# Kernel tuning notes

Hardware: AMD Instinct MI355X
Metric: run time of the kernel (lower is better)

Reference implementation:

```python
import jax, jax.numpy as jnp
import numpy as np

DIM = 1024
HEADS = 16
DIM_HEAD = 64
INNER = HEADS * DIM_HEAD  # 1024
EPS = 1e-5


def layernorm(x, w, b):
    mu = jnp.mean(x, axis=-1, keepdims=True)
    var = jnp.mean(jnp.square(x - mu), axis=-1, keepdims=True)
    return (x - mu) * jax.lax.rsqrt(var + EPS) * w + b


def setup_inputs() -> dict:
    key = jax.random.key(0)
    ks = jax.random.split(key, 9)
    b, n1, n2 = 4, 4096, 256
    x = jax.random.normal(ks[0], (b, n1, DIM), dtype=jnp.float32)
    latents = jax.random.normal(ks[1], (b, n2, DIM), dtype=jnp.float32)
    shift = jax.random.normal(ks[2], (b, HEADS), dtype=jnp.float32)
    scale = jax.random.normal(ks[3], (b, HEADS), dtype=jnp.float32)
    s = 1.0 / np.sqrt(DIM)
    Wq = jax.random.normal(ks[4], (DIM, INNER), dtype=jnp.float32) * s
    Wkv = jax.random.normal(ks[5], (DIM, 2 * INNER), dtype=jnp.float32) * s
    Wout = jax.random.normal(ks[6], (INNER, DIM), dtype=jnp.float32) * (1.0 / np.sqrt(INNER))
    ln1_w = jnp.ones((DIM,), jnp.float32)
    ln1_b = jnp.zeros((DIM,), jnp.float32)
    ln2_w = jnp.ones((DIM,), jnp.float32)
    ln2_b = jnp.zeros((DIM,), jnp.float32)
    return {"x": x, "latents": latents, "shift": shift, "scale": scale,
            "ln1_w": ln1_w, "ln1_b": ln1_b, "ln2_w": ln2_w, "ln2_b": ln2_b,
            "Wq": Wq, "Wkv": Wkv, "Wout": Wout}


def reference(x, latents, shift, scale, ln1_w, ln1_b, ln2_w, ln2_b, Wq, Wkv, Wout):
    b = x.shape[0]
    xn = layernorm(x, ln1_w, ln1_b)            # (b, n1, D)
    ln = layernorm(latents, ln2_w, ln2_b)      # (b, n2, D)
    q = ln @ Wq                                 # (b, n2, inner)
    kv = xn @ Wkv                               # (b, n1, 2*inner)
    k, v = jnp.split(kv, 2, axis=-1)
    q = q.reshape(b, -1, HEADS, DIM_HEAD)
    k = k.reshape(b, -1, HEADS, DIM_HEAD)
    v = v.reshape(b, -1, HEADS, DIM_HEAD)
    # AdaLN-style per-head modulation on q
    q = q * (1.0 + scale[:, None, :, None]) + shift[:, None, :, None]
    # fp32 attention scores (already fp32 here)
    attn_scale = DIM_HEAD ** -0.5
    qk = jnp.einsum('bihd,bjhd->bhij', q.astype(jnp.float32), k.astype(jnp.float32)) * attn_scale
    attn = jax.nn.softmax(qk, axis=-1).astype(v.dtype)  # (b, h, n2, n1)
    out = jnp.einsum('bhij,bjhd->bihd', attn, v)         # (b, n2, h, dh)
    out = out.reshape(b, -1, INNER)
    return out @ Wout
```

## Files before the change

kernel.cpp:

```cpp
#include <hip/hip_runtime.h>

typedef __bf16 bf16;
typedef bf16 bf16x8 __attribute__((ext_vector_type(8)));
typedef bf16 bf16x4 __attribute__((ext_vector_type(4)));
typedef float f32x4 __attribute__((ext_vector_type(4)));

#define B_ 4
#define N1 4096
#define N2 256
#define DIM 1024
#define HEADS 16
#define DH 64
#define INNER 1024
#define ASPLIT 4
#define KEYS_PER_SPLIT (N1 / ASPLIT)
#define SPLIT_ELEMS (4 * 16 * 256 * 64)
#define ROWS_TOTAL (4 * HEADS * N2)

typedef __attribute__((address_space(1))) const void gvoid_t;
typedef __attribute__((address_space(3))) void lvoid_t;
__device__ __forceinline__ void async16(const void* g, void* l) {
  __builtin_amdgcn_global_load_lds((gvoid_t*)g, (lvoid_t*)l, 16, 0, 0);
}

__global__ __launch_bounds__(256) void prep(
    const float* __restrict__ Wq, const float* __restrict__ Wkv,
    const float* __restrict__ Wout, bf16* __restrict__ WqT,
    bf16* __restrict__ WkvT, bf16* __restrict__ WoutT,
    const float* __restrict__ x, const float* __restrict__ latents,
    const float* __restrict__ ln1w, const float* __restrict__ ln1b,
    const float* __restrict__ ln2w, const float* __restrict__ ln2b,
    bf16* __restrict__ xn, bf16* __restrict__ lnl) {
  __shared__ float tile[32][33];
  int t = blockIdx.x;
  if (t < 4096) {
    const float* src;
    bf16* dst;
    int N;
    if (t < 1024) { src = Wq; dst = WqT; N = 1024; }
    else if (t < 3072) { t -= 1024; src = Wkv; dst = WkvT; N = 2048; }
    else { t -= 3072; src = Wout; dst = WoutT; N = 1024; }
    int ntiles = N >> 5;
    int n0 = (t % ntiles) * 32, k0 = (t / ntiles) * 32;
    int xx = threadIdx.x & 31, yy = threadIdx.x >> 5;
    for (int j = 0; j < 4; j++)
      tile[yy + 8 * j][xx] = src[(size_t)(k0 + yy + 8 * j) * N + n0 + xx];
    __syncthreads();
    for (int j = 0; j < 4; j++)
      dst[(size_t)(n0 + yy + 8 * j) * 1024 + k0 + xx] = (bf16)tile[xx][yy + 8 * j];
    return;
  }
  int wv = threadIdx.x >> 6, lane = threadIdx.x & 63;
  int grow = (t - 4096) * 4 + wv;
  const float *src, *w, *bb;
  bf16* dst;
  int row;
  if (grow < 16384) { src = x; w = ln1w; bb = ln1b; dst = xn; row = grow; }
  else { src = latents; w = ln2w; bb = ln2b; dst = lnl; row = grow - 16384; }
  const float4* p = (const float4*)(src + (size_t)row * DIM);
  float4 v[4];
  for (int j = 0; j < 4; j++) v[j] = p[j * 64 + lane];
  float s = 0.f, sq = 0.f;
  for (int j = 0; j < 4; j++) {
    s += v[j].x + v[j].y + v[j].z + v[j].w;
    sq += v[j].x * v[j].x + v[j].y * v[j].y + v[j].z * v[j].z + v[j].w * v[j].w;
  }
  for (int off = 32; off; off >>= 1) {
    s += __shfl_xor(s, off, 64);
    sq += __shfl_xor(sq, off, 64);
  }
  float mu = s * (1.0f / DIM);
  float var = sq * (1.0f / DIM) - mu * mu;
  float r = rsqrtf(var + 1e-5f);
  for (int j = 0; j < 4; j++) {
    float4 wv4 = ((const float4*)w)[j * 64 + lane];
    float4 bv4 = ((const float4*)bb)[j * 64 + lane];
    bf16x4 o;
    o[0] = (bf16)((v[j].x - mu) * r * wv4.x + bv4.x);
    o[1] = (bf16)((v[j].y - mu) * r * wv4.y + bv4.y);
    o[2] = (bf16)((v[j].z - mu) * r * wv4.z + bv4.z);
    o[3] = (bf16)((v[j].w - mu) * r * wv4.w + bv4.w);
    *(bf16x4*)(dst + (size_t)row * DIM + (j * 64 + lane) * 4) = o;
  }
}

__device__ __forceinline__ int swz_off(int row, int cb) {
  int line = row >> 1;
  return (line << 7) + (((((row & 1) << 2) | cb) ^ (line & 7)) << 4);
}

__global__ __launch_bounds__(512, 2) void gemm_kv256(
    const bf16* __restrict__ A, const bf16* __restrict__ Bt,
    bf16* __restrict__ Cout, bf16* __restrict__ Cout2) {
  extern __shared__ char smem[];
  int tid = threadIdx.x;
  int lane = tid & 63, wv = tid >> 6;
  int lr = lane & 15, quad = lane >> 4;
  int wr = wv >> 2, wc = wv & 3;
  int bid = blockIdx.x;
  int mt = (bid & 7) * 8 + ((bid >> 3) >> 3), nt = (bid >> 3) & 7;
  int m0 = mt * 256, n0 = nt * 256;

  int offA[8], offB[4];
#pragma unroll
  for (int im = 0; im < 8; im++) offA[im] = swz_off(wr * 128 + im * 16 + lr, quad);
#pragma unroll
  for (int in = 0; in < 4; in++) offB[in] = swz_off(wc * 64 + in * 16 + lr, quad);

  size_t gA[2], gB[2];
#pragma unroll
  for (int s = 0; s < 2; s++) {
    int u = s * 512 + tid;
    int line = u >> 3, inner = (u & 7) ^ (line & 7);
    int row = line * 2 + (inner >> 2), cb = inner & 3;
    gA[s] = (size_t)(m0 + row) * 1024 + cb * 8;
    gB[s] = (size_t)(n0 + row) * 1024 + cb * 8;
  }
  int ldsS0 = wv * 1024, ldsS1 = 8192 + wv * 1024;

  auto stA = [&](int b, int kh, int k0) {
    char* base = smem + b * 32768 + kh * 16384;
    async16(&A[gA[0] + k0], base + ldsS0);
    async16(&A[gA[1] + k0], base + ldsS1);
  };
  auto stB = [&](int b, int kh, int k0) {
    char* base = smem + 65536 + b * 32768 + kh * 16384;
    async16(&Bt[gB[0] + k0], base + ldsS0);
    async16(&Bt[gB[1] + k0], base + ldsS1);
  };

  f32x4 acc[8][4] = {};

  stA(0, 0, 0);  stB(0, 0, 0);
  stA(0, 1, 32); stB(0, 1, 32);
  stA(1, 0, 64); stB(1, 0, 64);
  asm volatile("s_waitcnt vmcnt(4)" ::: "memory");
  __builtin_amdgcn_s_barrier();

#pragma unroll 1
  for (int t = 0; t < 16; t++) {
    int b = t & 1;
    const char* A0 = smem + b * 32768;
    const char* A1 = A0 + 16384;
    const char* B0 = smem + 65536 + b * 32768;
    const char* B1 = B0 + 16384;
    int k1 = (t + 1 < 16 ? t + 1 : 15) * 64;
    int k2 = (t + 2 < 16 ? t + 2 : 15) * 64;
    bf16x8 af[4], bfr[4];
#pragma unroll
    for (int in = 0; in < 4; in++) bfr[in] = *(const bf16x8*)(B0 + offB[in]);
#pragma unroll
    for (int im = 0; im < 4; im++) af[im] = *(const bf16x8*)(A0 + offA[im]);
    stA(b ^ 1, 1, k1 + 32);
    __builtin_amdgcn_s_barrier();
    __builtin_amdgcn_s_setprio(1);
#pragma unroll
    for (int im = 0; im < 4; im++)
#pragma unroll
      for (int in = 0; in < 4; in++)
        acc[im][in] = __builtin_amdgcn_mfma_f32_16x16x32_bf16(
            af[im], bfr[in], acc[im][in], 0, 0, 0);
    __builtin_amdgcn_s_setprio(0);
    __builtin_amdgcn_s_barrier();
#pragma unroll
    for (int im = 0; im < 4; im++) af[im] = *(const bf16x8*)(A0 + offA[4 + im]);
    stB(b ^ 1, 1, k1 + 32);
    __builtin_amdgcn_s_barrier();
    __builtin_amdgcn_s_setprio(1);
#pragma unroll
    for (int im = 0; im < 4; im++)
#pragma unroll
      for (int in = 0; in < 4; in++)
        acc[4 + im][in] = __builtin_amdgcn_mfma_f32_16x16x32_bf16(
            af[im], bfr[in], acc[4 + im][in], 0, 0, 0);
    __builtin_amdgcn_s_setprio(0);
    __builtin_amdgcn_s_barrier();
#pragma unroll
    for (int in = 0; in < 4; in++) bfr[in] = *(const bf16x8*)(B1 + offB[in]);
#pragma unroll
    for (int im = 0; im < 4; im++) af[im] = *(const bf16x8*)(A1 + offA[im]);
    stA(b, 0, k2);
    __builtin_amdgcn_s_barrier();
    __builtin_amdgcn_s_setprio(1);
#pragma unroll
    for (int im = 0; im < 4; im++)
#pragma unroll
      for (int in = 0; in < 4; in++)
        acc[im][in] = __builtin_amdgcn_mfma_f32_16x16x32_bf16(
            af[im], bfr[in], acc[im][in], 0, 0, 0);
    __builtin_amdgcn_s_setprio(0);
    __builtin_amdgcn_s_barrier();
#pragma unroll
    for (int im = 0; im < 4; im++) af[im] = *(const bf16x8*)(A1 + offA[4 + im]);
    stB(b, 0, k2);
    __builtin_amdgcn_s_barrier();
    __builtin_amdgcn_s_setprio(1);
#pragma unroll
    for (int im = 0; im < 4; im++)
#pragma unroll
      for (int in = 0; in < 4; in++)
        acc[4 + im][in] = __builtin_amdgcn_mfma_f32_16x16x32_bf16(
            af[im], bfr[in], acc[4 + im][in], 0, 0, 0);
    __builtin_amdgcn_s_setprio(0);
    asm volatile("s_waitcnt vmcnt(4)" ::: "memory");
    __builtin_amdgcn_s_barrier();
  }

  asm volatile("s_waitcnt vmcnt(0)" ::: "memory");
  __builtin_amdgcn_s_barrier();

  if (n0 < 1024) {
#pragma unroll
    for (int im = 0; im < 8; im++)
#pragma unroll
      for (int in = 0; in < 4; in++) {
        int col = n0 + wc * 64 + in * 16 + lr;
#pragma unroll
        for (int r = 0; r < 4; r++) {
          int row = m0 + wr * 128 + im * 16 + quad * 4 + r;
          Cout[(size_t)row * 1024 + col] = (bf16)acc[im][in][r];
        }
      }
    return;
  }
  int b2 = m0 >> 12;
  int key0 = (m0 & 4095) + wr * 128;
  int gc0 = (n0 - 1024) + wc * 64;
  bf16* Tw = (bf16*)(smem + wv * 8704);
  for (int pass = 0; pass < 2; pass++) {
#pragma unroll
    for (int ii = 0; ii < 2; ii++) {
      int in = pass * 2 + ii;
      int cl = ii * 16 + lr;
#pragma unroll
      for (int im = 0; im < 8; im++) {
        bf16x4 pk;
#pragma unroll
        for (int r = 0; r < 4; r++) pk[r] = (bf16)acc[im][in][r];
        *(bf16x4*)&Tw[cl * 136 + im * 16 + quad * 4] = pk;
      }
    }
    asm volatile("s_waitcnt lgkmcnt(0)" ::: "memory");
#pragma unroll
    for (int j = 0; j < 8; j++) {
      int idx = j * 64 + lane;
      int cl = idx >> 4, k8 = idx & 15;
      uint4 val = *(const uint4*)&Tw[cl * 136 + k8 * 8];
      *(uint4*)&Cout2[((size_t)(b2 * 1024 + gc0 + pass * 32 + cl)) * 4096 +
                      key0 + k8 * 8] = val;
    }
    asm volatile("s_waitcnt lgkmcnt(0)" ::: "memory");
  }
}

template <int MODE>
__global__ __launch_bounds__(256) void gemm64(
    const bf16* __restrict__ A, const bf16* __restrict__ Bt,
    void* __restrict__ Cout, int K, int N,
    const float* __restrict__ shiftp, const float* __restrict__ scalep) {
  __shared__ __align__(16) bf16 As[3][64 * 64];
  __shared__ __align__(16) bf16 Bs[3][64 * 64];
  int tid = threadIdx.x;
  int lane = tid & 63, wv = tid >> 6;
  int wr = wv >> 1, wc = wv & 1;
  int quad = lane >> 4, lr = lane & 15;
  int m0 = blockIdx.y * 64, n0 = blockIdx.x * 64;
  f32x4 acc[2][2] = {};

  auto stage = [&](int step, int buf) {
    int kt = step * 64;
    for (int j = 0; j < 2; j++) {
      int idx0 = j * 256 + wv * 64;
      int row = (idx0 >> 3) + (lane >> 3);
      int cb = (lane & 7) ^ (row & 7);
      async16(&A[(size_t)(m0 + row) * K + kt + cb * 8], &As[buf][idx0 * 8]);
      async16(&Bt[(size_t)(n0 + row) * K + kt + cb * 8], &Bs[buf][idx0 * 8]);
    }
  };

  int nsteps = K >> 6;
  stage(0, 0);
  stage(1, 1);
  asm volatile("s_waitcnt vmcnt(4)" ::: "memory");
  __builtin_amdgcn_s_barrier();

#pragma unroll 1
  for (int s = 0; s < nsteps; s++) {
    int cur = s % 3;
    int nxt = (s + 2 < nsteps) ? s + 2 : nsteps - 1;
    stage(nxt, (s + 2) % 3);
    for (int kk = 0; kk < 2; kk++) {
      bf16x8 af[2], bfr[2];
      for (int im = 0; im < 2; im++) {
        int row = wr * 32 + im * 16 + lr;
        af[im] =
            *(const bf16x8*)&As[cur][row * 64 + ((quad + 4 * kk) ^ (row & 7)) * 8];
      }
      for (int in = 0; in < 2; in++) {
        int row = wc * 32 + in * 16 + lr;
        bfr[in] =
            *(const bf16x8*)&Bs[cur][row * 64 + ((quad + 4 * kk) ^ (row & 7)) * 8];
      }
      for (int im = 0; im < 2; im++)
        for (int in = 0; in < 2; in++)
          acc[im][in] = __builtin_amdgcn_mfma_f32_16x16x32_bf16(
              af[im], bfr[in], acc[im][in], 0, 0, 0);
    }
    asm volatile("s_waitcnt vmcnt(4)" ::: "memory");
    __builtin_amdgcn_s_barrier();
  }

  for (int im = 0; im < 2; im++)
    for (int in = 0; in < 2; in++) {
      int col = n0 + wc * 32 + in * 16 + lr;
      for (int r = 0; r < 4; r++) {
        int row = m0 + wr * 32 + im * 16 + quad * 4 + r;
        float v = acc[im][in][r];
        if (MODE == 1) {
          int bb = row >> 8, hh = col >> 6;
          float sc = scalep[bb * 16 + hh], sh = shiftp[bb * 16 + hh];
          ((bf16*)Cout)[(size_t)row * N + col] =
              (bf16)((v * (1.0f + sc) + sh) * 0.18033688011112042f);
        } else {
          ((float*)Cout)[(size_t)row * N + col] = v;
        }
      }
    }
}

__global__ __launch_bounds__(512) void attn_kernel(const bf16* __restrict__ q,
                                                   const bf16* __restrict__ kb,
                                                   const bf16* __restrict__ vt,
                                                   bf16* __restrict__ opb,
                                                   float* __restrict__ lseb) {
  int b = blockIdx.z, h = blockIdx.y;
  int sp = blockIdx.x;
  int tid = threadIdx.x, lane = tid & 63, wv = tid >> 6;
  int quad = lane >> 4, lr = lane & 15;
  __shared__ __align__(16) bf16 Ks[2][64 * 64];
  __shared__ __align__(16) bf16 Vs[2][64 * 64];
  __shared__ __align__(16) bf16 QP[256 * 64];

  const bf16* qg = q + (size_t)(b * N2) * INNER + h * DH;
  for (int j = 0; j < 4; j++) {
    int r0 = j * 64 + wv * 8;
    int r = r0 + (lane >> 3);
    async16(&qg[(size_t)r * INNER + ((lane & 7) ^ (r & 7)) * 8], &QP[r0 * 64]);
  }
  __syncthreads();
  bf16x8 aQ[2][2];
  for (int g = 0; g < 2; g++) {
    int row = wv * 32 + g * 16 + lr;
    for (int kk = 0; kk < 2; kk++)
      aQ[g][kk] = *(const bf16x8*)&QP[row * 64 + ((quad + 4 * kk) ^ (row & 7)) * 8];
  }
  float m_s[2] = {-1e30f, -1e30f}, l_s[2] = {0.0f, 0.0f};
  f32x4 oacc[2][4] = {};

  const bf16* kg = kb + (size_t)(b * N1) * 1024 + h * DH;
  const bf16* vg = vt + (size_t)((b * HEADS + h) * DH) * N1;
  bf16* Ps = QP + wv * 2048;

  auto stageKV = [&](int t, int buf) {
    int key0 = sp * KEYS_PER_SPLIT + t * 64;
    int r0 = wv * 8;
    int r = r0 + (lane >> 3);
    int cs = ((lane & 7) ^ (r & 7)) * 8;
    async16(&kg[(size_t)(key0 + r) * 1024 + cs], &Ks[buf][r0 * 64]);
    async16(&vg[(size_t)r * N1 + key0 + cs], &Vs[buf][r0 * 64]);
  };

  stageKV(0, 0);
  asm volatile("s_waitcnt vmcnt(0)" ::: "memory");
  __builtin_amdgcn_s_barrier();

  for (int t = 0; t < KEYS_PER_SPLIT / 64; t++) {
    int cur = t & 1;
    bf16x8 ak[2][4], bv[2][4];
    for (int kk = 0; kk < 2; kk++)
      for (int nt = 0; nt < 4; nt++) {
        int row = nt * 16 + lr;
        ak[kk][nt] =
            *(const bf16x8*)&Ks[cur][row * 64 + ((quad + 4 * kk) ^ (row & 7)) * 8];
        bv[kk][nt] =
            *(const bf16x8*)&Vs[cur][row * 64 + ((quad + 4 * kk) ^ (row & 7)) * 8];
      }
    if (t + 1 < KEYS_PER_SPLIT / 64) stageKV(t + 1, cur ^ 1);

    for (int g = 0; g < 2; g++) {
      f32x4 s[4] = {};
      for (int kk = 0; kk < 2; kk++)
        for (int nt = 0; nt < 4; nt++)
          s[nt] = __builtin_amdgcn_mfma_f32_16x16x32_bf16(ak[kk][nt], aQ[g][kk],
                                                          s[nt], 0, 0, 0);
      float mx = s[0][0];
      for (int nt = 0; nt < 4; nt++)
        for (int r = 0; r < 4; r++) mx = fmaxf(mx, s[nt][r]);
      mx = fmaxf(mx, __shfl_xor(mx, 16, 64));
      mx = fmaxf(mx, __shfl_xor(mx, 32, 64));
      float mo = m_s[g];
      float mn = fmaxf(mo, mx);
      float al = exp2f(mo - mn);
      float p[4][4], sum = 0.0f;
      for (int nt = 0; nt < 4; nt++)
        for (int r = 0; r < 4; r++) {
          p[nt][r] = exp2f(s[nt][r] - mn);
          sum += p[nt][r];
        }
      sum += __shfl_xor(sum, 16, 64);
      sum += __shfl_xor(sum, 32, 64);
      l_s[g] = l_s[g] * al + sum;
      m_s[g] = mn;

      for (int nt = 0; nt < 4; nt++) {
        bf16x4 pk;
        for (int r = 0; r < 4; r++) pk[r] = (bf16)p[nt][r];
        *(bf16x4*)&Ps[lr * 64 + ((2 * nt + (quad >> 1)) ^ (lr & 7)) * 8 +
                      (quad & 1) * 4] = pk;
      }

      if (__any(mn > mo)) {
        for (int r = 0; r < 4; r++) {
          float a = __shfl(al, quad * 4 + r, 16);
          for (int in = 0; in < 4; in++) oacc[g][in][r] *= a;
        }
      }

      bf16x8 aP[2];
      for (int kk = 0; kk < 2; kk++)
        aP[kk] = *(const bf16x8*)&Ps[lr * 64 + ((4 * kk + quad) ^ (lr & 7)) * 8];
      for (int kk = 0; kk < 2; kk++)
        for (int in = 0; in < 4; in++)
          oacc[g][in] = __builtin_amdgcn_mfma_f32_16x16x32_bf16(
              aP[kk], bv[kk][in], oacc[g][in], 0, 0, 0);
    }
    asm volatile("s_waitcnt vmcnt(0)" ::: "memory");
    __builtin_amdgcn_s_barrier();
  }

  bf16* ob = opb + (size_t)sp * SPLIT_ELEMS;
  size_t rbase = (size_t)(b * HEADS + h) * N2;
  for (int g = 0; g < 2; g++) {
    for (int r = 0; r < 4; r++) {
      float lrow = __shfl(l_s[g], quad * 4 + r, 16);
      float inv = 1.0f / lrow;
      int qq = wv * 32 + g * 16 + quad * 4 + r;
      for (int in = 0; in < 4; in++)
        ob[(rbase + qq) * 64 + in * 16 + lr] = (bf16)(oacc[g][in][r] * inv);
    }
    if (quad == 0) {
      int qq = wv * 32 + g * 16 + lr;
      lseb[(size_t)sp * ROWS_TOTAL + rbase + qq] = m_s[g] + __log2f(l_s[g]);
    }
  }
}

__global__ __launch_bounds__(256) void combine_kernel(const bf16* __restrict__ opb,
                                                      const float* __restrict__ lseb,
                                                      bf16* __restrict__ out) {
  int gid = blockIdx.x * 256 + threadIdx.x;
  int dc = (gid & 7) * 8;
  int rq = gid >> 3;
  int qq = rq & 255, bh = rq >> 8;
  int h = bh & 15, b = bh >> 4;
  float ls[ASPLIT];
  for (int s = 0; s < ASPLIT; s++) ls[s] = lseb[(size_t)s * ROWS_TOTAL + rq];
  float M = fmaxf(fmaxf(ls[0], ls[1]), fmaxf(ls[2], ls[3]));
  float L = 0.0f, w[ASPLIT];
  for (int s = 0; s < ASPLIT; s++) {
    w[s] = exp2f(ls[s] - M);
    L += w[s];
  }
  float inv = 1.0f / L;
  float o[8] = {};
  for (int s = 0; s < ASPLIT; s++) {
    bf16x8 v = *(const bf16x8*)&opb[(size_t)s * SPLIT_ELEMS + (size_t)rq * 64 + dc];
    for (int j = 0; j < 8; j++) o[j] += w[s] * (float)v[j];
  }
  bf16x8 ov;
  for (int j = 0; j < 8; j++) ov[j] = (bf16)(o[j] * inv);
  *(bf16x8*)&out[((size_t)(b * N2 + qq)) * INNER + h * DH + dc] = ov;
}

extern "C" void kernel_launch(void* const* d_in, const int* in_sizes, int n_in,
                              void* d_out, int out_size, void* d_ws,
                              size_t ws_size, hipStream_t stream) {
  const float* x       = (const float*)d_in[0];
  const float* latents = (const float*)d_in[1];
  const float* shift   = (const float*)d_in[2];
  const float* scale   = (const float*)d_in[3];
  const float* ln1w    = (const float*)d_in[4];
  const float* ln1b    = (const float*)d_in[5];
  const float* ln2w    = (const float*)d_in[6];
  const float* ln2b    = (const float*)d_in[7];
  const float* Wq      = (const float*)d_in[8];
  const float* Wkv     = (const float*)d_in[9];
  const float* Wout    = (const float*)d_in[10];

  char* ws = (char*)d_ws;
  bf16*  xn    = (bf16*)(ws);
  bf16*  opb   = (bf16*)(ws);
  bf16*  lnl   = (bf16*)(ws + 33554432);
  float* lseb  = (float*)(ws + 33554432);
  bf16*  qb    = (bf16*)(ws + 35651584);
  bf16*  kb    = (bf16*)(ws + 37748736);
  bf16*  vtb   = (bf16*)(ws + 104857600);
  bf16*  aob   = (bf16*)(ws + 138412032);
  bf16*  WqT   = (bf16*)(ws + 140509184);
  bf16*  WkvT  = (bf16*)(ws + 142606336);
  bf16*  WoutT = (bf16*)(ws + 146800640);

  static bool attr_done = false;
  if (!attr_done) {
    hipFuncSetAttribute(reinterpret_cast<const void*>(gemm_kv256),
                        hipFuncAttributeMaxDynamicSharedMemorySize, 131072);
    attr_done = true;
  }

  prep<<<8448, 256, 0, stream>>>(Wq, Wkv, Wout, WqT, WkvT, WoutT, x, latents,
                                 ln1w, ln1b, ln2w, ln2b, xn, lnl);
  gemm_kv256<<<dim3(512), dim3(512), 131072, stream>>>(xn, WkvT, kb, vtb);
  gemm64<1><<<dim3(16, 16), 256, 0, stream>>>(lnl, WqT, qb, 1024, 1024, shift,
                                              scale);
  attn_kernel<<<dim3(ASPLIT, 16, 4), 512, 0, stream>>>(qb, kb, vtb, opb,
                                                       lseb);
  combine_kernel<<<512, 256, 0, stream>>>(opb, lseb, aob);
  gemm64<2><<<dim3(16, 16), 256, 0, stream>>>(aob, WoutT, d_out, 1024, 1024,
                                              nullptr, nullptr);
}
```

Before: 265.7 us.

## Fold Q projection GEMM into KV GEMM launch as extra blocks

Appends 256 extra blocks to the KV GEMM kernel, and each computes a 64x64 tile of the Q projection with AdaLN modulation and the attention scale. This removes the separate gemm64<1> launch and lets the Q work fill idle CUs alongside the big KV GEMM. The Q blocks use a 512-thread block and a small 3-stage LDS pipeline, so they inherit the 128KB dynamic shared memory allocation and may limit occupancy. The 0.18 scale constant suggests the softmax now works in base 2, so consumers must match.

```diff
diff --git a/kernel.cpp b/kernel.cpp
--- a/kernel.cpp
+++ b/kernel.cpp
@@ -91,13 +91,72 @@
 
 __global__ __launch_bounds__(512, 2) void gemm_kv256(
     const bf16* __restrict__ A, const bf16* __restrict__ Bt,
-    bf16* __restrict__ Cout, bf16* __restrict__ Cout2) {
+    bf16* __restrict__ Cout, bf16* __restrict__ Cout2,
+    const bf16* __restrict__ Aq, const bf16* __restrict__ Bq,
+    bf16* __restrict__ qout, const float* __restrict__ shiftp,
+    const float* __restrict__ scalep) {
   extern __shared__ char smem[];
   int tid = threadIdx.x;
   int lane = tid & 63, wv = tid >> 6;
   int lr = lane & 15, quad = lane >> 4;
+  int bid = blockIdx.x;
+
+  if (bid >= 512) {
+    int q2 = bid - 512;
+    int m0q = (q2 >> 4) * 64, n0q = (q2 & 15) * 64;
+    int wrq = wv >> 1, wcq = wv & 1;
+    int srow = tid >> 3;
+    int scb = (tid & 7) ^ (srow & 7);
+    size_t ga = (size_t)(m0q + srow) * 1024 + scb * 8;
+    size_t gb = (size_t)(n0q + srow) * 1024 + scb * 8;
+    int ldsW = wv * 1024;
+    auto stq = [&](int step, int buf) {
+      int kt = step * 64;
+      async16(&Aq[ga + kt], smem + buf * 8192 + ldsW);
+      async16(&Bq[gb + kt], smem + 24576 + buf * 8192 + ldsW);
+    };
+    f32x4 accq[2] = {};
+    stq(0, 0);
+    stq(1, 1);
+    asm volatile("s_waitcnt vmcnt(2)" ::: "memory");
+    __builtin_amdgcn_s_barrier();
+#pragma unroll 1
+    for (int s = 0; s < 16; s++) {
+      int cur = s % 3;
+      int nxt = (s + 2 < 16) ? s + 2 : 15;
+      stq(nxt, (s + 2) % 3);
+      const bf16* Ab = (const bf16*)(smem + cur * 8192);
+      const bf16* Bb = (const bf16*)(smem + 24576 + cur * 8192);
+      for (int kk = 0; kk < 2; kk++) {
+        int arow = wrq * 16 + lr;
+        bf16x8 afq =
+            *(const bf16x8*)&Ab[arow * 64 + ((4 * kk + quad) ^ (arow & 7)) * 8];
+        for (int in = 0; in < 2; in++) {
+          int brow = wcq * 32 + in * 16 + lr;
+          bf16x8 bfq =
+              *(const bf16x8*)&Bb[brow * 64 + ((4 * kk + quad) ^ (brow & 7)) * 8];
+          accq[in] = __builtin_amdgcn_mfma_f32_16x16x32_bf16(afq, bfq, accq[in],
+                                                             0, 0, 0);
+        }
+      }
+      asm volatile("s_waitcnt vmcnt(2)" ::: "memory");
+      __builtin_amdgcn_s_barrier();
+    }
+    for (int in = 0; in < 2; in++) {
+      int col = n0q + wcq * 32 + in * 16 + lr;
+      int hh = col >> 6;
+      for (int r = 0; r < 4; r++) {
+        int row = m0q + wrq * 16 + quad * 4 + r;
+        int bb = row >> 8;
+        float sc = scalep[bb * 16 + hh], sh = shiftp[bb * 16 + hh];
+        qout[(size_t)row * 1024 + col] =
+            (bf16)((accq[in][r] * (1.0f + sc) + sh) * 0.18033688011112042f);
+      }
+    }
+    return;
+  }
+
   int wr = wv >> 2, wc = wv & 3;
-  int bid = blockIdx.x;
   int mt = (bid & 7) * 8 + ((bid >> 3) >> 3), nt = (bid >> 3) & 7;
   int m0 = mt * 256, n0 = nt * 256;
 
@@ -519,9 +578,8 @@
 
   prep<<<8448, 256, 0, stream>>>(Wq, Wkv, Wout, WqT, WkvT, WoutT, x, latents,
                                  ln1w, ln1b, ln2w, ln2b, xn, lnl);
-  gemm_kv256<<<dim3(512), dim3(512), 131072, stream>>>(xn, WkvT, kb, vtb);
-  gemm64<1><<<dim3(16, 16), 256, 0, stream>>>(lnl, WqT, qb, 1024, 1024, shift,
-                                              scale);
+  gemm_kv256<<<dim3(768), dim3(512), 131072, stream>>>(
+      xn, WkvT, kb, vtb, lnl, WqT, qb, shift, scale);
   attn_kernel<<<dim3(ASPLIT, 16, 4), 512, 0, stream>>>(qb, kb, vtb, opb,
                                                        lseb);
   combine_kernel<<<512, 256, 0, stream>>>(opb, lseb, aob);
```

Result: no change. 262.8 us (median of 3 runs) (-1.1%).
